# Kernel optimization log

Measured on AMD Instinct MI355X. Metric: run time of the kernel, lower is better.

Reference implementation:

```python
import jax, jax.numpy as jnp
import numpy as np


def _gru(x_seq, W_ih, W_hh, b_ih, b_hh):
    """Batched torch-style GRU. x_seq: [B,T,H] -> outputs [B,T,H].
    Gate order (torch.nn.GRU): r, z, n. n = tanh(xn + r*(W_hn h + b_hn))."""
    B, T, H = x_seq.shape
    # precompute input projections for all timesteps: [B,T,3H]
    xp = jnp.einsum('bth,gh->btg', x_seq, W_ih) + b_ih

    def step(h, xt):  # h: [B,H], xt: [B,3H]
        hp = h @ W_hh.T + b_hh  # [B,3H]
        xr, xz, xn = jnp.split(xt, 3, axis=-1)
        hr, hz, hn = jnp.split(hp, 3, axis=-1)
        r = jax.nn.sigmoid(xr + hr)
        z = jax.nn.sigmoid(xz + hz)
        n = jnp.tanh(xn + r * hn)
        h_new = (1.0 - z) * n + z * h
        return h_new, h_new

    h0 = jnp.zeros((B, H), dtype=x_seq.dtype)
    _, hs = jax.lax.scan(step, h0, jnp.swapaxes(xp, 0, 1))  # [T,B,H]
    return jnp.swapaxes(hs, 0, 1)


def setup_inputs() -> dict:
    key = jax.random.key(0)
    B, T, C, H, D = 128, 64, 8000, 256, 16
    G = 3 * H
    ks = jax.random.split(key, 32)
    s = 0.05  # scale for stable params
    inp = {
        'x': (jax.random.uniform(ks[0], (B, T, C)) < 0.01).astype(jnp.float32),  # sparse multi-hot
        'demographic': jax.random.normal(ks[1], (B, D), jnp.float32),
        'embed_W': jax.random.normal(ks[2], (H, C), jnp.float32) * s,
        'embed_b': jax.random.normal(ks[3], (H,), jnp.float32) * s,
        'aW_ih': jax.random.normal(ks[4], (G, H), jnp.float32) * s,
        'aW_hh': jax.random.normal(ks[5], (G, H), jnp.float32) * s,
        'ab_ih': jax.random.normal(ks[6], (G,), jnp.float32) * s,
        'ab_hh': jax.random.normal(ks[7], (G,), jnp.float32) * s,
        'bW_ih': jax.random.normal(ks[8], (G, H), jnp.float32) * s,
        'bW_hh': jax.random.normal(ks[9], (G, H), jnp.float32) * s,
        'bb_ih': jax.random.normal(ks[10], (G,), jnp.float32) * s,
        'bb_hh': jax.random.normal(ks[11], (G,), jnp.float32) * s,
        'attnA_W': jax.random.normal(ks[12], (1, H), jnp.float32) * s,
        'attnA_b': jax.random.normal(ks[13], (1,), jnp.float32) * s,
        'attnB_W': jax.random.normal(ks[14], (H, H), jnp.float32) * s,
        'attnB_b': jax.random.normal(ks[15], (H,), jnp.float32) * s,
        'cls_W1': jax.random.normal(ks[16], (H, H + D), jnp.float32) * s,
        'cls_b1': jax.random.normal(ks[17], (H,), jnp.float32) * s,
        'cls_W2': jax.random.normal(ks[18], (C, H), jnp.float32) * s,
        'cls_b2': jax.random.normal(ks[19], (C,), jnp.float32) * s,
        'dl_W1': jax.random.normal(ks[20], (H, H + D), jnp.float32) * s,
        'dl_b1': jax.random.normal(ks[21], (H,), jnp.float32) * s,
        'dl_W2': jax.random.normal(ks[22], (1, H), jnp.float32) * s,
        'dl_b2': jax.random.normal(ks[23], (1,), jnp.float32) * s,
    }
    return inp


def reference(x, demographic, embed_W, embed_b,
              aW_ih, aW_hh, ab_ih, ab_hh,
              bW_ih, bW_hh, bb_ih, bb_hh,
              attnA_W, attnA_b, attnB_W, attnB_b,
              cls_W1, cls_b1, cls_W2, cls_b2,
              dl_W1, dl_b1, dl_W2, dl_b2):
    # code embedding: [B,T,C] @ [C,H] -> [B,T,H]
    embedded = jnp.einsum('btc,hc->bth', x, embed_W) + embed_b

    alpha_out = _gru(embedded, aW_ih, aW_hh, ab_ih, ab_hh)  # [B,T,H]
    beta_out = _gru(embedded, bW_ih, bW_hh, bb_ih, bb_hh)   # [B,T,H]

    e_alpha = jnp.einsum('bth,oh->bto', alpha_out, attnA_W)[..., 0] + attnA_b[0]  # [B,T]
    alpha = jax.nn.softmax(e_alpha, axis=1)                                       # [B,T]
    beta = jnp.tanh(jnp.einsum('bth,gh->btg', beta_out, attnB_W) + attnB_b)       # [B,T,H]

    context = jnp.einsum('bth,bt->bh', embedded * beta, alpha)  # [B,H]

    combined = jnp.concatenate([context, demographic], axis=1)  # [B,H+D]
    # classifier (dropout = identity, eval mode)
    h1 = jax.nn.relu(combined @ cls_W1.T + cls_b1)
    logits = h1 @ cls_W2.T + cls_b2                              # [B,C]
    # death/LOS head
    h2 = jax.nn.relu(combined @ dl_W1.T + dl_b1)
    dl_logit = h2 @ dl_W2.T + dl_b2                              # [B,1]

    return jnp.concatenate([logits, dl_logit], axis=1)          # [B,C+1]
```

## Files before the change

### kernel.cpp

```cpp
#include <hip/hip_runtime.h>


typedef __attribute__((ext_vector_type(4))) float f32x4;
typedef __attribute__((ext_vector_type(8))) short short8;

__device__ inline short f2bf(float f) {
  unsigned u = __float_as_uint(f);
  u += 0x7fffu + ((u >> 16) & 1u);
  return (short)(u >> 16);
}
__device__ inline float bf2f(short u) {
  return __uint_as_float(((unsigned)(unsigned short)u) << 16);
}
__device__ inline float sigf(float x) { return 1.f / (1.f + __expf(-x)); }
__device__ inline float tanh_fast(float x) {
  x = fminf(fmaxf(x, -15.f), 15.f);
  float e = __expf(2.f * x);
  return (e - 1.f) / (e + 1.f);
}

__global__ void transpose_w(const float* __restrict__ in, float* __restrict__ outT) {
  __shared__ float tile[32][33];
  const int tx = threadIdx.x, ty = threadIdx.y;
  const int c0 = blockIdx.x * 32, h0 = blockIdx.y * 32;
#pragma unroll
  for (int k = 0; k < 4; ++k)
    tile[ty * 4 + k][tx] = in[(long)(h0 + ty * 4 + k) * 8000 + c0 + tx];
  __syncthreads();
#pragma unroll
  for (int k = 0; k < 4; ++k)
    outT[(long)(c0 + ty * 4 + k) * 256 + h0 + tx] = tile[tx][ty * 4 + k];
}

__global__ __launch_bounds__(512) void pad_pack(const float* __restrict__ w1,
                                                const float* __restrict__ w1d,
                                                float* __restrict__ o1,
                                                float* __restrict__ o2,
                                                const float* __restrict__ aWhh,
                                                const float* __restrict__ bWhh,
                                                short* __restrict__ wbf,
                                                const float* __restrict__ aWih,
                                                const float* __restrict__ bWih,
                                                const float* __restrict__ attnBW,
                                                short* __restrict__ wih16a,
                                                short* __restrict__ wih16b,
                                                short* __restrict__ attnBW16) {
  const int bid = blockIdx.x;
  if (bid < 288) {
    int idx = bid * 512 + threadIdx.x;
    int half = idx / (256 * 288);
    int r = idx % (256 * 288);
    int n = r / 288, k = r % 288;
    float v = (k < 272) ? (half ? w1d[n * 272 + k] : w1[n * 272 + k]) : 0.f;
    if (half) o2[r] = v; else o1[r] = v;
  } else if (bid < 384) {
    const int F = (bid - 288) * 512 + threadIdx.x;
    int f = F;
    const int lane = f & 63; f >>= 6;
    const int w = f & 15; f >>= 4;
    const int e = f % 3; f /= 3;
    const int kt = f & 7; f >>= 3;
    const int gru = f;
    const float* W = gru ? bWhh : aWhh;
    const int g = e * 256 + w * 16 + (lane & 15);
    const int k = kt * 32 + (lane >> 4) * 8;
    const float* p = W + (long)g * 256 + k;
    short8 v;
#pragma unroll
    for (int j = 0; j < 8; ++j) v[j] = f2bf(p[j]);
    *(short8*)(wbf + (long)F * 8) = v;
  } else {
    const int i = (bid - 384) * 512 + threadIdx.x;
    if (i < 196608) wih16a[i] = f2bf(aWih[i]);
    else if (i < 393216) wih16b[i - 196608] = f2bf(bWih[i - 196608]);
    else attnBW16[i - 393216] = f2bf(attnBW[i - 393216]);
  }
}

__global__ __launch_bounds__(256) void embed_sparse(const float* __restrict__ x,
                                                    const float* __restrict__ Wt,
                                                    const float* __restrict__ eb,
                                                    short* __restrict__ emb16) {
  __shared__ int sidx[512];
  __shared__ float sval[512];
  __shared__ int scnt;
  const int bt = blockIdx.x;
  const int tid = threadIdx.x;
  if (tid == 0) scnt = 0;
  __syncthreads();
  const float* xr = x + (long)bt * 8000;
  for (int i = tid; i < 2000; i += 256) {
    float4 v = ((const float4*)xr)[i];
    if (v.x != 0.f) { int p = atomicAdd(&scnt, 1); if (p < 512) { sidx[p] = i * 4 + 0; sval[p] = v.x; } }
    if (v.y != 0.f) { int p = atomicAdd(&scnt, 1); if (p < 512) { sidx[p] = i * 4 + 1; sval[p] = v.y; } }
    if (v.z != 0.f) { int p = atomicAdd(&scnt, 1); if (p < 512) { sidx[p] = i * 4 + 2; sval[p] = v.z; } }
    if (v.w != 0.f) { int p = atomicAdd(&scnt, 1); if (p < 512) { sidx[p] = i * 4 + 3; sval[p] = v.w; } }
  }
  __syncthreads();
  const int n = min(scnt, 512);
  float acc = eb[tid];
  for (int i = 0; i < n; ++i) acc += sval[i] * Wt[(long)sidx[i] * 256 + tid];
  emb16[(long)bt * 256 + tid] = f2bf(acc);
}

__global__ __launch_bounds__(256) void gemm_bt(const float* __restrict__ A,
                                               const float* __restrict__ B,
                                               const float* __restrict__ bias,
                                               float* __restrict__ C,
                                               int M, int N, int K, int ldc, int act) {
  __shared__ short As[64][40];
  __shared__ short Bs[64][40];
  const int tid = threadIdx.x;
  const int lane = tid & 63, wave = tid >> 6;
  const int wm = wave >> 1, wn = wave & 1;
  const int l15 = lane & 15, lhi = lane >> 4;
  const int m0 = blockIdx.y * 64, n0 = blockIdx.x * 64;
  const int srow = tid >> 2, scol = (tid & 3) * 8;
  f32x4 acc[2][2];
#pragma unroll
  for (int i = 0; i < 2; ++i)
#pragma unroll
    for (int j = 0; j < 2; ++j) acc[i][j] = (f32x4){0.f, 0.f, 0.f, 0.f};

  for (int k0 = 0; k0 < K; k0 += 32) {
    __syncthreads();
    {
      const float* p = A + (long)(m0 + srow) * K + k0 + scol;
      float4 f0 = *(const float4*)p;
      float4 f1 = *(const float4*)(p + 4);
      short8 v;
      v[0] = f2bf(f0.x); v[1] = f2bf(f0.y); v[2] = f2bf(f0.z); v[3] = f2bf(f0.w);
      v[4] = f2bf(f1.x); v[5] = f2bf(f1.y); v[6] = f2bf(f1.z); v[7] = f2bf(f1.w);
      *(short8*)&As[srow][scol] = v;
      const float* q = B + (long)(n0 + srow) * K + k0 + scol;
      float4 g0 = *(const float4*)q;
      float4 g1 = *(const float4*)(q + 4);
      short8 u;
      u[0] = f2bf(g0.x); u[1] = f2bf(g0.y); u[2] = f2bf(g0.z); u[3] = f2bf(g0.w);
      u[4] = f2bf(g1.x); u[5] = f2bf(g1.y); u[6] = f2bf(g1.z); u[7] = f2bf(g1.w);
      *(short8*)&Bs[srow][scol] = u;
    }
    __syncthreads();
    short8 af0 = *(const short8*)&As[wm * 32 + l15][lhi * 8];
    short8 af1 = *(const short8*)&As[wm * 32 + 16 + l15][lhi * 8];
    short8 bf0 = *(const short8*)&Bs[wn * 32 + l15][lhi * 8];
    short8 bf1 = *(const short8*)&Bs[wn * 32 + 16 + l15][lhi * 8];
    acc[0][0] = __builtin_amdgcn_mfma_f32_16x16x32_bf16(af0, bf0, acc[0][0], 0, 0, 0);
    acc[0][1] = __builtin_amdgcn_mfma_f32_16x16x32_bf16(af0, bf1, acc[0][1], 0, 0, 0);
    acc[1][0] = __builtin_amdgcn_mfma_f32_16x16x32_bf16(af1, bf0, acc[1][0], 0, 0, 0);
    acc[1][1] = __builtin_amdgcn_mfma_f32_16x16x32_bf16(af1, bf1, acc[1][1], 0, 0, 0);
  }
#pragma unroll
  for (int j = 0; j < 2; ++j) {
    const int col = n0 + wn * 32 + j * 16 + l15;
    const float bv = bias[col];
#pragma unroll
    for (int i = 0; i < 2; ++i) {
#pragma unroll
      for (int r = 0; r < 4; ++r) {
        const int row = m0 + wm * 32 + i * 16 + lhi * 4 + r;
        float v = acc[i][j][r] + bv;
        if (act == 1) v = fmaxf(v, 0.f);
        else if (act == 2) v = tanh_fast(v);
        C[(long)row * ldc + col] = v;
      }
    }
  }
}

__global__ __launch_bounds__(256) void gemm_dual16(const short* __restrict__ A,
                                                   const short* __restrict__ B1,
                                                   const short* __restrict__ B2,
                                                   const float* __restrict__ bias1,
                                                   const float* __restrict__ bias2,
                                                   short* __restrict__ C1,
                                                   short* __restrict__ C2,
                                                   int K) {
  __shared__ short As[64][40];
  __shared__ short Bs1[64][40];
  __shared__ short Bs2[64][40];
  const int tid = threadIdx.x;
  const int lane = tid & 63, wave = tid >> 6;
  const int wm = wave >> 1, wn = wave & 1;
  const int l15 = lane & 15, lhi = lane >> 4;
  const int m0 = blockIdx.y * 64, n0 = blockIdx.x * 64;
  const int srow = tid >> 2, scol = (tid & 3) * 8;
  f32x4 acc1[2][2], acc2[2][2];
#pragma unroll
  for (int i = 0; i < 2; ++i)
#pragma unroll
    for (int j = 0; j < 2; ++j) {
      acc1[i][j] = (f32x4){0.f, 0.f, 0.f, 0.f};
      acc2[i][j] = (f32x4){0.f, 0.f, 0.f, 0.f};
    }

  for (int k0 = 0; k0 < K; k0 += 32) {
    __syncthreads();
    {
      *(short8*)&As[srow][scol]  = *(const short8*)(A  + (long)(m0 + srow) * K + k0 + scol);
      *(short8*)&Bs1[srow][scol] = *(const short8*)(B1 + (long)(n0 + srow) * K + k0 + scol);
      *(short8*)&Bs2[srow][scol] = *(const short8*)(B2 + (long)(n0 + srow) * K + k0 + scol);
    }
    __syncthreads();
    short8 af0 = *(const short8*)&As[wm * 32 + l15][lhi * 8];
    short8 af1 = *(const short8*)&As[wm * 32 + 16 + l15][lhi * 8];
    short8 b10 = *(const short8*)&Bs1[wn * 32 + l15][lhi * 8];
    short8 b11 = *(const short8*)&Bs1[wn * 32 + 16 + l15][lhi * 8];
    short8 b20 = *(const short8*)&Bs2[wn * 32 + l15][lhi * 8];
    short8 b21 = *(const short8*)&Bs2[wn * 32 + 16 + l15][lhi * 8];
    acc1[0][0] = __builtin_amdgcn_mfma_f32_16x16x32_bf16(af0, b10, acc1[0][0], 0, 0, 0);
    acc1[0][1] = __builtin_amdgcn_mfma_f32_16x16x32_bf16(af0, b11, acc1[0][1], 0, 0, 0);
    acc1[1][0] = __builtin_amdgcn_mfma_f32_16x16x32_bf16(af1, b10, acc1[1][0], 0, 0, 0);
    acc1[1][1] = __builtin_amdgcn_mfma_f32_16x16x32_bf16(af1, b11, acc1[1][1], 0, 0, 0);
    acc2[0][0] = __builtin_amdgcn_mfma_f32_16x16x32_bf16(af0, b20, acc2[0][0], 0, 0, 0);
    acc2[0][1] = __builtin_amdgcn_mfma_f32_16x16x32_bf16(af0, b21, acc2[0][1], 0, 0, 0);
    acc2[1][0] = __builtin_amdgcn_mfma_f32_16x16x32_bf16(af1, b20, acc2[1][0], 0, 0, 0);
    acc2[1][1] = __builtin_amdgcn_mfma_f32_16x16x32_bf16(af1, b21, acc2[1][1], 0, 0, 0);
  }
#pragma unroll
  for (int j = 0; j < 2; ++j) {
    const int col = n0 + wn * 32 + j * 16 + l15;
    const float bv1 = bias1[col];
    const float bv2 = bias2[col];
#pragma unroll
    for (int i = 0; i < 2; ++i) {
#pragma unroll
      for (int r = 0; r < 4; ++r) {
        const int row = m0 + wm * 32 + i * 16 + lhi * 4 + r;
        C1[(long)row * 768 + col] = f2bf(acc1[i][j][r] + bv1);
        C2[(long)row * 768 + col] = f2bf(acc2[i][j][r] + bv2);
      }
    }
  }
}

__global__ __launch_bounds__(256) void gemm16_bt(const short* __restrict__ A,
                                                 const short* __restrict__ B,
                                                 const float* __restrict__ bias,
                                                 float* __restrict__ C,
                                                 int N_, int K, int ldc, int act) {
  __shared__ short As[64][40];
  __shared__ short Bs[64][40];
  const int tid = threadIdx.x;
  const int lane = tid & 63, wave = tid >> 6;
  const int wm = wave >> 1, wn = wave & 1;
  const int l15 = lane & 15, lhi = lane >> 4;
  const int m0 = blockIdx.y * 64, n0 = blockIdx.x * 64;
  const int srow = tid >> 2, scol = (tid & 3) * 8;
  f32x4 acc[2][2];
#pragma unroll
  for (int i = 0; i < 2; ++i)
#pragma unroll
    for (int j = 0; j < 2; ++j) acc[i][j] = (f32x4){0.f, 0.f, 0.f, 0.f};

  for (int k0 = 0; k0 < K; k0 += 32) {
    __syncthreads();
    {
      *(short8*)&As[srow][scol] = *(const short8*)(A + (long)(m0 + srow) * K + k0 + scol);
      *(short8*)&Bs[srow][scol] = *(const short8*)(B + (long)(n0 + srow) * K + k0 + scol);
    }
    __syncthreads();
    short8 af0 = *(const short8*)&As[wm * 32 + l15][lhi * 8];
    short8 af1 = *(const short8*)&As[wm * 32 + 16 + l15][lhi * 8];
    short8 bf0 = *(const short8*)&Bs[wn * 32 + l15][lhi * 8];
    short8 bf1 = *(const short8*)&Bs[wn * 32 + 16 + l15][lhi * 8];
    acc[0][0] = __builtin_amdgcn_mfma_f32_16x16x32_bf16(af0, bf0, acc[0][0], 0, 0, 0);
    acc[0][1] = __builtin_amdgcn_mfma_f32_16x16x32_bf16(af0, bf1, acc[0][1], 0, 0, 0);
    acc[1][0] = __builtin_amdgcn_mfma_f32_16x16x32_bf16(af1, bf0, acc[1][0], 0, 0, 0);
    acc[1][1] = __builtin_amdgcn_mfma_f32_16x16x32_bf16(af1, bf1, acc[1][1], 0, 0, 0);
  }
#pragma unroll
  for (int j = 0; j < 2; ++j) {
    const int col = n0 + wn * 32 + j * 16 + l15;
    const float bv = bias[col];
#pragma unroll
    for (int i = 0; i < 2; ++i) {
#pragma unroll
      for (int r = 0; r < 4; ++r) {
        const int row = m0 + wm * 32 + i * 16 + lhi * 4 + r;
        float v = acc[i][j][r] + bv;
        if (act == 1) v = fmaxf(v, 0.f);
        else if (act == 2) v = tanh_fast(v);
        C[(long)row * ldc + col] = v;
      }
    }
  }
  (void)N_;
}

__global__ __launch_bounds__(1024, 4)
void gru_scan(const short* __restrict__ xpa,
              const short* __restrict__ xpb,
              const short* __restrict__ wbf,
              const float* __restrict__ abhh,
              const float* __restrict__ bbhh,
              short* __restrict__ aout,
              short* __restrict__ bout) {
  const int tid = threadIdx.x;
  const int lane = tid & 63, w = tid >> 6;
  const int l15 = lane & 15, lhi = lane >> 4;
  const int gru = blockIdx.x >> 5, chunk = blockIdx.x & 31;
  const int b0 = chunk * 4;
  const short* xp  = gru ? xpb : xpa;
  const float* bhh = gru ? bbhh : abhh;
  short* outp = gru ? bout : aout;

  __shared__ short hl[2][16][264];
  __shared__ short xplb[2][4][768];
  __shared__ short wlds[16][3][64][8];

  auto FR = [&](int kt, int e) -> const short8* {
    return (const short8*)(wbf + ((((long)gru * 8 + kt) * 3 + e) * 16 + w) * 512 + (long)lane * 8);
  };

  short8 wf[3][5];
#pragma unroll
  for (int e = 0; e < 3; ++e)
#pragma unroll
    for (int kt = 0; kt < 5; ++kt) wf[e][kt] = *FR(kt, e);
#pragma unroll
  for (int e = 0; e < 3; ++e) *(short8*)&wlds[w][e][lane][0] = *FR(5, e);

  float bh[3];
#pragma unroll
  for (int e = 0; e < 3; ++e) bh[e] = bhh[e * 256 + w * 16 + l15];

  for (int i = tid; i < 2 * 16 * 264; i += 1024) (&hl[0][0][0])[i] = 0;

  auto STAGE = [&](int par, int tt) {
    if (w < 6) {
      const int c = w * 64 + lane;
      const int b = c / 96, off8 = (c % 96) * 8;
      const short* gp = xp + ((long)(b0 + b) * 64 + tt) * 768 + off8;
      __builtin_amdgcn_global_load_lds((const __attribute__((address_space(1))) unsigned int*)gp,
                                       (__attribute__((address_space(3))) unsigned int*)((short*)&xplb[par][0][0] + (long)w * 512),
                                       16, 0, 0);
    }
  };
  STAGE(0, 0);
  __syncthreads();

  float hreg = 0.f;
  const int col = w * 16 + l15;

  for (int t = 0; t < 64; ++t) {
    const int cur = t & 1;
    short8 s60 = *FR(6, 0), s61 = *FR(6, 1), s62 = *FR(6, 2);
    short8 s70 = *FR(7, 0), s71 = *FR(7, 1), s72 = *FR(7, 2);
    if (t + 1 < 64) STAGE(cur ^ 1, t + 1);

    f32x4 acc[3];
#pragma unroll
    for (int e = 0; e < 3; ++e) acc[e] = (f32x4){0.f, 0.f, 0.f, 0.f};
#pragma unroll
    for (int kt = 0; kt < 5; ++kt) {
      short8 a = *(const short8*)&hl[cur][l15][kt * 32 + lhi * 8];
      acc[0] = __builtin_amdgcn_mfma_f32_16x16x32_bf16(a, wf[0][kt], acc[0], 0, 0, 0);
      acc[1] = __builtin_amdgcn_mfma_f32_16x16x32_bf16(a, wf[1][kt], acc[1], 0, 0, 0);
      acc[2] = __builtin_amdgcn_mfma_f32_16x16x32_bf16(a, wf[2][kt], acc[2], 0, 0, 0);
    }
    {
      short8 a = *(const short8*)&hl[cur][l15][5 * 32 + lhi * 8];
#pragma unroll
      for (int e = 0; e < 3; ++e) {
        short8 wl = *(const short8*)&wlds[w][e][lane][0];
        acc[e] = __builtin_amdgcn_mfma_f32_16x16x32_bf16(a, wl, acc[e], 0, 0, 0);
      }
    }
    {
      short8 a = *(const short8*)&hl[cur][l15][6 * 32 + lhi * 8];
      acc[0] = __builtin_amdgcn_mfma_f32_16x16x32_bf16(a, s60, acc[0], 0, 0, 0);
      acc[1] = __builtin_amdgcn_mfma_f32_16x16x32_bf16(a, s61, acc[1], 0, 0, 0);
      acc[2] = __builtin_amdgcn_mfma_f32_16x16x32_bf16(a, s62, acc[2], 0, 0, 0);
    }
    {
      short8 a = *(const short8*)&hl[cur][l15][7 * 32 + lhi * 8];
      acc[0] = __builtin_amdgcn_mfma_f32_16x16x32_bf16(a, s70, acc[0], 0, 0, 0);
      acc[1] = __builtin_amdgcn_mfma_f32_16x16x32_bf16(a, s71, acc[1], 0, 0, 0);
      acc[2] = __builtin_amdgcn_mfma_f32_16x16x32_bf16(a, s72, acc[2], 0, 0, 0);
    }

    {
      const float xr = bf2f(xplb[cur][lhi][col]);
      const float xz = bf2f(xplb[cur][lhi][256 + col]);
      const float xn = bf2f(xplb[cur][lhi][512 + col]);
      const float r = sigf(xr + acc[0][0] + bh[0]);
      const float z = sigf(xz + acc[1][0] + bh[1]);
      const float n = tanh_fast(xn + r * (acc[2][0] + bh[2]));
      const float hn = (1.f - z) * n + z * hreg;
      hreg = hn;
      const short hb = f2bf(hn);
      hl[cur ^ 1][lhi << 2][col] = hb;
      outp[((long)(b0 + lhi) * 64 + t) * 256 + col] = hb;
    }
    __syncthreads();
  }
}

__global__ __launch_bounds__(256) void alpha_ctx(const short* __restrict__ aout16,
                                                 const float* __restrict__ aW,
                                                 const float* __restrict__ ab,
                                                 const short* __restrict__ emb16,
                                                 const float* __restrict__ beta,
                                                 const float* __restrict__ demo,
                                                 float* __restrict__ comb) {
  __shared__ float part[64][4];
  __shared__ float al[64];
  const int b = blockIdx.x, tid = threadIdx.x;
  const int t = tid >> 2, q = tid & 3;
  const short* p = aout16 + (long)(b * 64 + t) * 256 + q * 64;
  const float* wv = aW + q * 64;
  float s = 0.f;
  for (int i = 0; i < 64; ++i) s += bf2f(p[i]) * wv[i];
  part[t][q] = s;
  __syncthreads();
  if (tid < 64) {
    float e = part[tid][0] + part[tid][1] + part[tid][2] + part[tid][3] + ab[0];
    float m = e;
    for (int k = 32; k; k >>= 1) m = fmaxf(m, __shfl_xor(m, k));
    float ex = __expf(e - m);
    float sum = ex;
    for (int k = 32; k; k >>= 1) sum += __shfl_xor(sum, k);
    al[tid] = ex / sum;
  }
  __syncthreads();
  const int h = tid;
  float acc = 0.f;
  for (int t2 = 0; t2 < 64; ++t2) {
    const long ix = (long)(b * 64 + t2) * 256 + h;
    acc += al[t2] * bf2f(emb16[ix]) * beta[ix];
  }
  comb[b * 288 + h] = acc;
  if (h < 16) comb[b * 288 + 256 + h] = demo[b * 16 + h];
  else if (h < 32) comb[b * 288 + 256 + h] = 0.f;
}

__global__ __launch_bounds__(64) void dl_head(const float* __restrict__ h2,
                                              const float* __restrict__ w,
                                              const float* __restrict__ bias,
                                              float* __restrict__ out) {
  const int b = blockIdx.x, lane = threadIdx.x;
  float s = 0.f;
#pragma unroll
  for (int i = 0; i < 4; ++i) s += h2[b * 256 + lane * 4 + i] * w[lane * 4 + i];
  for (int k = 32; k; k >>= 1) s += __shfl_xor(s, k);
  if (lane == 0) out[(long)b * 8001 + 8000] = s + bias[0];
}

extern "C" void kernel_launch(void* const* d_in, const int* in_sizes, int n_in,
                              void* d_out, int out_size, void* d_ws, size_t ws_size,
                              hipStream_t stream) {
  (void)in_sizes; (void)n_in; (void)out_size; (void)ws_size;
  const float* x      = (const float*)d_in[0];
  const float* demo   = (const float*)d_in[1];
  const float* embW   = (const float*)d_in[2];
  const float* embB   = (const float*)d_in[3];
  const float* aWih   = (const float*)d_in[4];
  const float* aWhh   = (const float*)d_in[5];
  const float* abih   = (const float*)d_in[6];
  const float* abhh   = (const float*)d_in[7];
  const float* bWih   = (const float*)d_in[8];
  const float* bWhh   = (const float*)d_in[9];
  const float* bbih   = (const float*)d_in[10];
  const float* bbhh   = (const float*)d_in[11];
  const float* attnAW = (const float*)d_in[12];
  const float* attnAb = (const float*)d_in[13];
  const float* attnBW = (const float*)d_in[14];
  const float* attnBb = (const float*)d_in[15];
  const float* clsW1  = (const float*)d_in[16];
  const float* clsb1  = (const float*)d_in[17];
  const float* clsW2  = (const float*)d_in[18];
  const float* clsb2  = (const float*)d_in[19];
  const float* dlW1   = (const float*)d_in[20];
  const float* dlb1   = (const float*)d_in[21];
  const float* dlW2   = (const float*)d_in[22];
  const float* dlb2   = (const float*)d_in[23];
  float* out = (float*)d_out;
  float* ws = (float*)d_ws;

  float* Wt      = ws;
  short* emb16   = (short*)(Wt + 2048000);
  short* xpa16   = emb16 + 2097152;
  short* xpb16   = xpa16 + 6291456;
  short* aout16  = xpb16 + 6291456;
  short* bout16  = aout16 + 2097152;
  float* betaB   = (float*)(bout16 + 2097152);
  float* comb    = betaB + 2097152;
  float* h1      = comb + 36864;
  float* h2      = h1 + 32768;
  float* W1p     = h2 + 32768;
  float* W1pd    = W1p + 73728;
  short* wbf     = (short*)(W1pd + 73728);
  short* wih16a  = wbf + 393216;
  short* wih16b  = wih16a + 196608;
  short* attnBW16 = wih16b + 196608;

  transpose_w<<<dim3(250, 8), dim3(32, 8), 0, stream>>>(embW, Wt);
  pad_pack<<<dim3(1280), dim3(512), 0, stream>>>(clsW1, dlW1, W1p, W1pd, aWhh, bWhh, wbf,
                                                 aWih, bWih, attnBW, wih16a, wih16b, attnBW16);
  embed_sparse<<<dim3(8192), dim3(256), 0, stream>>>(x, Wt, embB, emb16);
  gemm_dual16<<<dim3(12, 128), dim3(256), 0, stream>>>(emb16, wih16a, wih16b, abih, bbih,
                                                       xpa16, xpb16, 256);
  gru_scan<<<dim3(64), dim3(1024), 0, stream>>>(xpa16, xpb16, wbf, abhh, bbhh, aout16, bout16);
  gemm16_bt<<<dim3(4, 128), dim3(256), 0, stream>>>(bout16, attnBW16, attnBb, betaB, 256, 256, 256, 2);
  alpha_ctx<<<dim3(128), dim3(256), 0, stream>>>(aout16, attnAW, attnAb, emb16, betaB, demo, comb);
  gemm_bt<<<dim3(4, 2), dim3(256), 0, stream>>>(comb, W1p, clsb1, h1, 128, 256, 288, 256, 1);
  gemm_bt<<<dim3(4, 2), dim3(256), 0, stream>>>(comb, W1pd, dlb1, h2, 128, 256, 288, 256, 1);
  gemm_bt<<<dim3(125, 2), dim3(256), 0, stream>>>(h1, clsW2, clsb2, out, 128, 8000, 256, 8001, 0);
  dl_head<<<dim3(128), dim3(64), 0, stream>>>(h2, dlW2, dlb2, out);
}
```

Baseline: 255.4 us.

## Prefetch GRU input projections into registers, relax scan barrier, store beta as bf16

The GRU scan no longer stages the per-step input projections into LDS through global_load_lds. Each lane now loads its three bf16 gate inputs for the next timestep straight into registers a step ahead. The full __syncthreads at the end of each step becomes an LDS-only waitcnt plus a raw s_barrier, so the per-step barrier no longer waits on outstanding global memory. The attention-beta GEMM now writes bf16 instead of fp32, which halves the beta traffic read by alpha_ctx at some cost in precision. The risk is that global-load latency now sits on the recurrent critical path if one step of prefetch is not enough to hide it.

```diff
diff --git a/kernel.cpp b/kernel.cpp
--- a/kernel.cpp
+++ b/kernel.cpp
@@ -237,8 +237,8 @@
 __global__ __launch_bounds__(256) void gemm16_bt(const short* __restrict__ A,
                                                  const short* __restrict__ B,
                                                  const float* __restrict__ bias,
-                                                 float* __restrict__ C,
-                                                 int N_, int K, int ldc, int act) {
+                                                 short* __restrict__ C,
+                                                 int K, int ldc) {
   __shared__ short As[64][40];
   __shared__ short Bs[64][40];
   const int tid = threadIdx.x;
@@ -278,14 +278,10 @@
 #pragma unroll
       for (int r = 0; r < 4; ++r) {
         const int row = m0 + wm * 32 + i * 16 + lhi * 4 + r;
-        float v = acc[i][j][r] + bv;
-        if (act == 1) v = fmaxf(v, 0.f);
-        else if (act == 2) v = tanh_fast(v);
-        C[(long)row * ldc + col] = v;
+        C[(long)row * ldc + col] = f2bf(tanh_fast(acc[i][j][r] + bv));
       }
     }
   }
-  (void)N_;
 }
 
 __global__ __launch_bounds__(1024, 4)
@@ -306,7 +302,6 @@
   short* outp = gru ? bout : aout;
 
   __shared__ short hl[2][16][264];
-  __shared__ short xplb[2][4][768];
   __shared__ short wlds[16][3][64][8];
 
   auto FR = [&](int kt, int e) -> const short8* {
@@ -327,27 +322,19 @@
 
   for (int i = tid; i < 2 * 16 * 264; i += 1024) (&hl[0][0][0])[i] = 0;
 
-  auto STAGE = [&](int par, int tt) {
-    if (w < 6) {
-      const int c = w * 64 + lane;
-      const int b = c / 96, off8 = (c % 96) * 8;
-      const short* gp = xp + ((long)(b0 + b) * 64 + tt) * 768 + off8;
-      __builtin_amdgcn_global_load_lds((const __attribute__((address_space(1))) unsigned int*)gp,
-                                       (__attribute__((address_space(3))) unsigned int*)((short*)&xplb[par][0][0] + (long)w * 512),
-                                       16, 0, 0);
-    }
-  };
-  STAGE(0, 0);
-  __syncthreads();
+  const int col = w * 16 + l15;
+  const short* xpl = xp + ((long)(b0 + lhi) * 64) * 768 + col;
 
   float hreg = 0.f;
-  const int col = w * 16 + l15;
+  short xc0 = xpl[0], xc1 = xpl[256], xc2 = xpl[512];
+  __syncthreads();
 
   for (int t = 0; t < 64; ++t) {
     const int cur = t & 1;
+    const short* xpn = xpl + (long)(t + 1 < 64 ? t + 1 : 63) * 768;
+    short xn0 = xpn[0], xn1 = xpn[256], xn2 = xpn[512];
     short8 s60 = *FR(6, 0), s61 = *FR(6, 1), s62 = *FR(6, 2);
     short8 s70 = *FR(7, 0), s71 = *FR(7, 1), s72 = *FR(7, 2);
-    if (t + 1 < 64) STAGE(cur ^ 1, t + 1);
 
     f32x4 acc[3];
 #pragma unroll
@@ -381,19 +368,20 @@
     }
 
     {
-      const float xr = bf2f(xplb[cur][lhi][col]);
-      const float xz = bf2f(xplb[cur][lhi][256 + col]);
-      const float xn = bf2f(xplb[cur][lhi][512 + col]);
-      const float r = sigf(xr + acc[0][0] + bh[0]);
-      const float z = sigf(xz + acc[1][0] + bh[1]);
-      const float n = tanh_fast(xn + r * (acc[2][0] + bh[2]));
+      const float r = sigf(bf2f(xc0) + acc[0][0] + bh[0]);
+      const float z = sigf(bf2f(xc1) + acc[1][0] + bh[1]);
+      const float n = tanh_fast(bf2f(xc2) + r * (acc[2][0] + bh[2]));
       const float hn = (1.f - z) * n + z * hreg;
       hreg = hn;
       const short hb = f2bf(hn);
       hl[cur ^ 1][lhi << 2][col] = hb;
       outp[((long)(b0 + lhi) * 64 + t) * 256 + col] = hb;
     }
-    __syncthreads();
+    xc0 = xn0; xc1 = xn1; xc2 = xn2;
+    asm volatile("s_waitcnt lgkmcnt(0)" ::: "memory");
+    __builtin_amdgcn_sched_barrier(0);
+    __builtin_amdgcn_s_barrier();
+    __builtin_amdgcn_sched_barrier(0);
   }
 }
 
@@ -401,7 +389,7 @@
                                                  const float* __restrict__ aW,
                                                  const float* __restrict__ ab,
                                                  const short* __restrict__ emb16,
-                                                 const float* __restrict__ beta,
+                                                 const short* __restrict__ beta16,
                                                  const float* __restrict__ demo,
                                                  float* __restrict__ comb) {
   __shared__ float part[64][4];
@@ -428,7 +416,7 @@
   float acc = 0.f;
   for (int t2 = 0; t2 < 64; ++t2) {
     const long ix = (long)(b * 64 + t2) * 256 + h;
-    acc += al[t2] * bf2f(emb16[ix]) * beta[ix];
+    acc += al[t2] * bf2f(emb16[ix]) * bf2f(beta16[ix]);
   }
   comb[b * 288 + h] = acc;
   if (h < 16) comb[b * 288 + 256 + h] = demo[b * 16 + h];
@@ -484,8 +472,8 @@
   short* xpb16   = xpa16 + 6291456;
   short* aout16  = xpb16 + 6291456;
   short* bout16  = aout16 + 2097152;
-  float* betaB   = (float*)(bout16 + 2097152);
-  float* comb    = betaB + 2097152;
+  short* beta16  = bout16 + 2097152;
+  float* comb    = (float*)(beta16 + 2097152);
   float* h1      = comb + 36864;
   float* h2      = h1 + 32768;
   float* W1p     = h2 + 32768;
@@ -502,8 +490,8 @@
   gemm_dual16<<<dim3(12, 128), dim3(256), 0, stream>>>(emb16, wih16a, wih16b, abih, bbih,
                                                        xpa16, xpb16, 256);
   gru_scan<<<dim3(64), dim3(1024), 0, stream>>>(xpa16, xpb16, wbf, abhh, bbhh, aout16, bout16);
-  gemm16_bt<<<dim3(4, 128), dim3(256), 0, stream>>>(bout16, attnBW16, attnBb, betaB, 256, 256, 256, 2);
-  alpha_ctx<<<dim3(128), dim3(256), 0, stream>>>(aout16, attnAW, attnAb, emb16, betaB, demo, comb);
+  gemm16_bt<<<dim3(4, 128), dim3(256), 0, stream>>>(bout16, attnBW16, attnBb, beta16, 256, 256);
+  alpha_ctx<<<dim3(128), dim3(256), 0, stream>>>(aout16, attnAW, attnAb, emb16, beta16, demo, comb);
   gemm_bt<<<dim3(4, 2), dim3(256), 0, stream>>>(comb, W1p, clsb1, h1, 128, 256, 288, 256, 1);
   gemm_bt<<<dim3(4, 2), dim3(256), 0, stream>>>(comb, W1pd, dlb1, h2, 128, 256, 288, 256, 1);
   gemm_bt<<<dim3(125, 2), dim3(256), 0, stream>>>(h1, clsW2, clsb2, out, 128, 8000, 256, 8001, 0);
```

Result: no change. 254.0 us (-0.5%).
